# Kernel optimization log

Hardware: AMD Instinct MI355X
Metric: run time of the kernel (lower is better)

The kernel has to match this reference:

```python
import jax, jax.numpy as jnp
import numpy as np
import math

CHANNELS = 128
NUM_NODES = 170
LENGTH = 12
BATCH = 128


def setup_inputs() -> dict:
    key = jax.random.key(0)
    k_x, k_es = jax.random.split(key)
    x = jax.random.normal(k_x, (BATCH, CHANNELS, NUM_NODES, LENGTH), dtype=jnp.float32)
    # xavier_uniform for E_s [channels, num_nodes]
    bound = math.sqrt(6.0 / (CHANNELS + NUM_NODES))
    E_s = jax.random.uniform(k_es, (CHANNELS, NUM_NODES), dtype=jnp.float32,
                             minval=-bound, maxval=bound)
    return {"x": x, "E_s": E_s}


def reference(x, E_s):
    # x: [B, C, N, T], E_s: [C, M] with M == N (num_nodes)
    # Note: the original also computes E_t = x * E_tod**2, which is dead code
    # (never used in the returned value), so it is omitted here.
    C = x.shape[1]
    # node embeddings: sum over channel and time -> [B, N, M]
    E_d = jnp.tanh(jnp.einsum('bcnt,cm->bnm', x, E_s))
    # node-node similarity: contract over the M (embedding) axis -> [B, N, N]
    scores = jax.nn.relu(jnp.einsum('bnm,bkm->bnk', E_d, E_d) / jnp.sqrt(jnp.float32(C)))
    A_adp = jax.nn.softmax(scores, axis=-1)  # [B, N, N]
    A_mean = A_adp.mean(axis=0)              # [N, N]
    return (A_mean > 0.5).astype(jnp.float32)
```

## Files before the change

### kernel.cpp

```cpp
#include <hip/hip_runtime.h>
#include <math.h>

#define NB 128
#define NC 128
#define NN 170
#define NT 12
#define MP 176
#define BSROW 196

#define ESP_SZ (NC * MP)
#define ED_SZ  (NB * NN * MP)
#define P_SZ   (NB * NN * MP)
#define PM_SZ  (8 * NN * NN)

__device__ __forceinline__ float fast_tanh(float x) {
    float cx = fminf(fmaxf(x, -15.f), 15.f);
    float e  = __expf(2.f * cx);
    return (e - 1.f) * __builtin_amdgcn_rcpf(e + 1.f);
}

__global__ __launch_bounds__(256) void k0_pad_es(const float* __restrict__ Es,
                                                 float* __restrict__ Esp) {
    int idx = blockIdx.x * 256 + threadIdx.x;
    if (idx < ESP_SZ) {
        int c = idx / MP, m = idx % MP;
        Esp[idx] = (m < NN) ? Es[c * NN + m] : 0.f;
    }
}

__global__ __launch_bounds__(256) void k2_fused(const float* __restrict__ x,
                                                const float* __restrict__ Esp,
                                                float* __restrict__ Ed) {
    const int b = blockIdx.y, n0 = blockIdx.x * 32;
    const int t = threadIdx.x, tx = t & 15, ty = t >> 4;
    __shared__ __align__(16) float As[16][36];
    __shared__ __align__(16) float Bs[16][BSROW];

    float acc[2][12] = {};
    for (int c0 = 0; c0 < NC; c0 += 16) {
        __syncthreads();
        {
            int c  = t >> 4;
            int nn = (t & 15) * 2;
            #pragma unroll
            for (int u = 0; u < 2; ++u) {
                int n = n0 + nn + u;
                float s = 0.f;
                if (n < NN) {
                    const float4* p = reinterpret_cast<const float4*>(
                        x + ((size_t)((b * NC + c0 + c) * NN) + n) * NT);
                    float4 f0 = p[0], f1 = p[1], f2 = p[2];
                    s = ((f0.x + f0.y) + (f0.z + f0.w))
                      + ((f1.x + f1.y) + (f1.z + f1.w))
                      + ((f2.x + f2.y) + (f2.z + f2.w));
                }
                As[c][nn + u] = s;
            }
        }
        #pragma unroll
        for (int it = 0; it < 3; ++it) {
            int idx = t + it * 256;
            int c = idx / 48, mq = idx - c * 48;
            float4 v = make_float4(0.f, 0.f, 0.f, 0.f);
            if (mq < 44)
                v = *reinterpret_cast<const float4*>(Esp + (c0 + c) * MP + mq * 4);
            *reinterpret_cast<float4*>(&Bs[c][mq * 4]) = v;
        }
        __syncthreads();
        #pragma unroll
        for (int cc = 0; cc < 16; ++cc) {
            float2 av = *reinterpret_cast<const float2*>(&As[cc][ty * 2]);
            float a[2] = {av.x, av.y};
            float bb[12];
            #pragma unroll
            for (int off = 0; off < 3; ++off) {
                float4 bv = *reinterpret_cast<const float4*>(&Bs[cc][tx * 4 + off * 64]);
                bb[off * 4 + 0] = bv.x; bb[off * 4 + 1] = bv.y;
                bb[off * 4 + 2] = bv.z; bb[off * 4 + 3] = bv.w;
            }
            #pragma unroll
            for (int ii = 0; ii < 2; ++ii)
                #pragma unroll
                for (int jj = 0; jj < 12; ++jj)
                    acc[ii][jj] = fmaf(a[ii], bb[jj], acc[ii][jj]);
        }
    }
    #pragma unroll
    for (int ii = 0; ii < 2; ++ii) {
        int n = n0 + ty * 2 + ii;
        if (n >= NN) continue;
        float* Erow = Ed + ((size_t)(b * NN + n)) * MP;
        #pragma unroll
        for (int off = 0; off < 3; ++off) {
            int m = tx * 4 + off * 64;
            if (m >= MP) continue;
            float4 v;
            v.x = fast_tanh(acc[ii][off * 4 + 0]);
            v.y = fast_tanh(acc[ii][off * 4 + 1]);
            v.z = fast_tanh(acc[ii][off * 4 + 2]);
            v.w = fast_tanh(acc[ii][off * 4 + 3]);
            *reinterpret_cast<float4*>(Erow + m) = v;
        }
    }
}

__global__ __launch_bounds__(256) void k3_scores(const float* __restrict__ Ed,
                                                 float* __restrict__ P) {
    const int b = blockIdx.y, r0 = blockIdx.x * 32;
    const int t = threadIdx.x, tx = t & 15, ty = t >> 4;
    __shared__ __align__(16) float Bs[16][BSROW];
    const float* __restrict__ Edb = Ed + (size_t)b * NN * MP;

    float acc[2][12] = {};
    for (int mc = 0; mc < MP; mc += 16) {
        __syncthreads();
        #pragma unroll
        for (int it = 0; it < 3; ++it) {
            int idx = t + it * 256;
            int k = idx >> 2, mq = idx & 3;
            float4 v = make_float4(0.f, 0.f, 0.f, 0.f);
            if (k < NN)
                v = *reinterpret_cast<const float4*>(Edb + (size_t)k * MP + mc + mq * 4);
            Bs[mq * 4 + 0][k] = v.x;
            Bs[mq * 4 + 1][k] = v.y;
            Bs[mq * 4 + 2][k] = v.z;
            Bs[mq * 4 + 3][k] = v.w;
        }
        __syncthreads();
        #pragma unroll
        for (int mm = 0; mm < 16; ++mm) {
            float2 av = *reinterpret_cast<const float2*>(&Bs[mm][r0 + ty * 2]);
            float a[2] = {av.x, av.y};
            float bb[12];
            #pragma unroll
            for (int off = 0; off < 3; ++off) {
                float4 bv = *reinterpret_cast<const float4*>(&Bs[mm][tx * 4 + off * 64]);
                bb[off * 4 + 0] = bv.x; bb[off * 4 + 1] = bv.y;
                bb[off * 4 + 2] = bv.z; bb[off * 4 + 3] = bv.w;
            }
            #pragma unroll
            for (int ii = 0; ii < 2; ++ii)
                #pragma unroll
                for (int jj = 0; jj < 12; ++jj)
                    acc[ii][jj] = fmaf(a[ii], bb[jj], acc[ii][jj]);
        }
    }

    const float scale = 0.08838834764831845f;
    #pragma unroll
    for (int ii = 0; ii < 2; ++ii) {
        int n = r0 + ty * 2 + ii;
        float vv[12];
        float mx = -1.f;
        #pragma unroll
        for (int jj = 0; jj < 12; ++jj) {
            int k = tx * 4 + (jj & 3) + (jj >> 2) * 64;
            float v = fmaxf(acc[ii][jj] * scale, 0.f);
            vv[jj] = (k < NN) ? v : -1.f;
            mx = fmaxf(mx, vv[jj]);
        }
        #pragma unroll
        for (int off = 8; off; off >>= 1) mx = fmaxf(mx, __shfl_xor(mx, off, 64));
        float ex[12], sum = 0.f;
        #pragma unroll
        for (int jj = 0; jj < 12; ++jj) {
            int k = tx * 4 + (jj & 3) + (jj >> 2) * 64;
            float e = (k < NN) ? __expf(vv[jj] - mx) : 0.f;
            ex[jj] = e;
            sum += e;
        }
        #pragma unroll
        for (int off = 8; off; off >>= 1) sum += __shfl_xor(sum, off, 64);
        float inv = 1.f / sum;
        if (n < NN) {
            float* Pr = P + ((size_t)(b * NN + n)) * MP;
            #pragma unroll
            for (int off = 0; off < 3; ++off) {
                int k = tx * 4 + off * 64;
                if (k >= MP) continue;
                float4 v;
                v.x = ex[off * 4 + 0] * inv; v.y = ex[off * 4 + 1] * inv;
                v.z = ex[off * 4 + 2] * inv; v.w = ex[off * 4 + 3] * inv;
                *reinterpret_cast<float4*>(Pr + k) = v;
            }
        }
    }
}

__global__ __launch_bounds__(256) void k4a_partial(const float* __restrict__ P,
                                                   float* __restrict__ Pm) {
    int p = blockIdx.x * 256 + threadIdx.x;
    if (p >= NN * NN) return;
    int n = p / NN, k = p - n * NN;
    const float* base = P + (size_t)blockIdx.y * 16 * NN * MP + (size_t)n * MP + k;
    float s = 0.f;
    #pragma unroll
    for (int b = 0; b < 16; ++b) s += base[(size_t)b * NN * MP];
    Pm[blockIdx.y * (NN * NN) + p] = s;
}

__global__ __launch_bounds__(256) void k4b_thresh(const float* __restrict__ Pm,
                                                  float* __restrict__ out) {
    int p = blockIdx.x * 256 + threadIdx.x;
    if (p >= NN * NN) return;
    float s = 0.f;
    #pragma unroll
    for (int g = 0; g < 8; ++g) s += Pm[g * (NN * NN) + p];
    out[p] = (s * (1.f / 128.f) > 0.5f) ? 1.f : 0.f;
}

extern "C" void kernel_launch(void* const* d_in, const int* in_sizes, int n_in,
                              void* d_out, int out_size, void* d_ws, size_t ws_size,
                              hipStream_t stream) {
    const float* x  = (const float*)d_in[0];
    const float* Es = (const float*)d_in[1];
    float* out = (float*)d_out;
    float* wsf = (float*)d_ws;

    float* Esp = wsf;
    float* Ed  = wsf + ESP_SZ;
    float* P   = wsf + ESP_SZ + ED_SZ;
    float* Pm  = wsf + ESP_SZ + ED_SZ + P_SZ;

    k0_pad_es<<<88, 256, 0, stream>>>(Es, Esp);
    k2_fused<<<dim3(6, 128), 256, 0, stream>>>(x, Esp, Ed);
    k3_scores<<<dim3(6, 128), 256, 0, stream>>>(Ed, P);
    k4a_partial<<<dim3(113, 8), 256, 0, stream>>>(P, Pm);
    k4b_thresh<<<113, 256, 0, stream>>>(Pm, out);
}
```

Measured before the change: 243.7 us.

## Compute similarity scores with fp16 MFMA and row-wise softmax via shared memory

Replaces the FP32 FMA-based E_d·E_dᵀ score kernel with one that converts E_d tiles to fp16 in shared memory and uses 16x16x32 MFMA instructions. Scores are staged in shared memory so each wave runs softmax over whole rows with full-wave shuffles. The aim is to cut the ALU cost of the batched NxN GEMM. The trade-off is fp16 rounding of inputs, which could flip threshold decisions near 0.5, plus extra shared-memory staging.

Measured after the change: 234.7 us. 1.04x faster.

```diff
diff --git a/kernel.cpp b/kernel.cpp
--- a/kernel.cpp
+++ b/kernel.cpp
@@ -12,6 +12,11 @@
 #define ED_SZ  (NB * NN * MP)
 #define P_SZ   (NB * NN * MP)
 #define PM_SZ  (8 * NN * NN)
+
+typedef _Float16 h8 __attribute__((ext_vector_type(8)));
+typedef _Float16 h4 __attribute__((ext_vector_type(4)));
+typedef __fp16   g2 __attribute__((ext_vector_type(2)));
+typedef float    f4 __attribute__((ext_vector_type(4)));
 
 __device__ __forceinline__ float fast_tanh(float x) {
     float cx = fminf(fmaxf(x, -15.f), 15.f);
@@ -104,86 +109,86 @@
     }
 }
 
-__global__ __launch_bounds__(256) void k3_scores(const float* __restrict__ Ed,
-                                                 float* __restrict__ P) {
+__global__ __launch_bounds__(256) void k3_scores_mfma(const float* __restrict__ Ed,
+                                                      float* __restrict__ P) {
     const int b = blockIdx.y, r0 = blockIdx.x * 32;
-    const int t = threadIdx.x, tx = t & 15, ty = t >> 4;
-    __shared__ __align__(16) float Bs[16][BSROW];
+    const int t = threadIdx.x;
+    const int lane = t & 63, wave = t >> 6;
+    const int l15 = lane & 15, quad = lane >> 4;
+
+    __shared__ __align__(16) _Float16 Eh[192 * 40];
+    __shared__ __align__(16) float    Sc[32 * 204];
+
     const float* __restrict__ Edb = Ed + (size_t)b * NN * MP;
 
-    float acc[2][12] = {};
-    for (int mc = 0; mc < MP; mc += 16) {
-        __syncthreads();
-        #pragma unroll
-        for (int it = 0; it < 3; ++it) {
+    f4 acc[2][3] = {};
+    for (int mc = 0; mc < 192; mc += 32) {
+        __syncthreads();
+        #pragma unroll
+        for (int it = 0; it < 6; ++it) {
             int idx = t + it * 256;
-            int k = idx >> 2, mq = idx & 3;
+            int row = idx >> 3, q = idx & 7;
             float4 v = make_float4(0.f, 0.f, 0.f, 0.f);
-            if (k < NN)
-                v = *reinterpret_cast<const float4*>(Edb + (size_t)k * MP + mc + mq * 4);
-            Bs[mq * 4 + 0][k] = v.x;
-            Bs[mq * 4 + 1][k] = v.y;
-            Bs[mq * 4 + 2][k] = v.z;
-            Bs[mq * 4 + 3][k] = v.w;
-        }
-        __syncthreads();
-        #pragma unroll
-        for (int mm = 0; mm < 16; ++mm) {
-            float2 av = *reinterpret_cast<const float2*>(&Bs[mm][r0 + ty * 2]);
-            float a[2] = {av.x, av.y};
-            float bb[12];
-            #pragma unroll
-            for (int off = 0; off < 3; ++off) {
-                float4 bv = *reinterpret_cast<const float4*>(&Bs[mm][tx * 4 + off * 64]);
-                bb[off * 4 + 0] = bv.x; bb[off * 4 + 1] = bv.y;
-                bb[off * 4 + 2] = bv.z; bb[off * 4 + 3] = bv.w;
+            int col = mc + q * 4;
+            if (row < NN && col < MP)
+                v = *reinterpret_cast<const float4*>(Edb + (size_t)row * MP + col);
+            g2 lo = __builtin_amdgcn_cvt_pkrtz(v.x, v.y);
+            g2 hi = __builtin_amdgcn_cvt_pkrtz(v.z, v.w);
+            h4 h;
+            h[0] = (_Float16)lo[0]; h[1] = (_Float16)lo[1];
+            h[2] = (_Float16)hi[0]; h[3] = (_Float16)hi[1];
+            *reinterpret_cast<h4*>(&Eh[row * 40 + q * 4]) = h;
+        }
+        __syncthreads();
+        const int ko = quad * 8;
+        h8 a0 = *reinterpret_cast<const h8*>(&Eh[(r0 + l15) * 40 + ko]);
+        h8 a1 = *reinterpret_cast<const h8*>(&Eh[(r0 + 16 + l15) * 40 + ko]);
+        #pragma unroll
+        for (int ci = 0; ci < 3; ++ci) {
+            int kc = (wave * 3 + ci) * 16 + l15;
+            h8 bf = *reinterpret_cast<const h8*>(&Eh[kc * 40 + ko]);
+            acc[0][ci] = __builtin_amdgcn_mfma_f32_16x16x32_f16(a0, bf, acc[0][ci], 0, 0, 0);
+            acc[1][ci] = __builtin_amdgcn_mfma_f32_16x16x32_f16(a1, bf, acc[1][ci], 0, 0, 0);
+        }
+    }
+
+    const float scale = 0.08838834764831845f;
+    #pragma unroll
+    for (int rt = 0; rt < 2; ++rt)
+        #pragma unroll
+        for (int ci = 0; ci < 3; ++ci) {
+            int col = (wave * 3 + ci) * 16 + l15;
+            #pragma unroll
+            for (int reg = 0; reg < 4; ++reg) {
+                int rloc = rt * 16 + quad * 4 + reg;
+                Sc[rloc * 204 + col] = fmaxf(acc[rt][ci][reg] * scale, 0.f);
             }
-            #pragma unroll
-            for (int ii = 0; ii < 2; ++ii)
-                #pragma unroll
-                for (int jj = 0; jj < 12; ++jj)
-                    acc[ii][jj] = fmaf(a[ii], bb[jj], acc[ii][jj]);
-        }
-    }
-
-    const float scale = 0.08838834764831845f;
-    #pragma unroll
-    for (int ii = 0; ii < 2; ++ii) {
-        int n = r0 + ty * 2 + ii;
-        float vv[12];
-        float mx = -1.f;
-        #pragma unroll
-        for (int jj = 0; jj < 12; ++jj) {
-            int k = tx * 4 + (jj & 3) + (jj >> 2) * 64;
-            float v = fmaxf(acc[ii][jj] * scale, 0.f);
-            vv[jj] = (k < NN) ? v : -1.f;
-            mx = fmaxf(mx, vv[jj]);
-        }
-        #pragma unroll
-        for (int off = 8; off; off >>= 1) mx = fmaxf(mx, __shfl_xor(mx, off, 64));
-        float ex[12], sum = 0.f;
-        #pragma unroll
-        for (int jj = 0; jj < 12; ++jj) {
-            int k = tx * 4 + (jj & 3) + (jj >> 2) * 64;
-            float e = (k < NN) ? __expf(vv[jj] - mx) : 0.f;
-            ex[jj] = e;
-            sum += e;
-        }
-        #pragma unroll
-        for (int off = 8; off; off >>= 1) sum += __shfl_xor(sum, off, 64);
-        float inv = 1.f / sum;
-        if (n < NN) {
-            float* Pr = P + ((size_t)(b * NN + n)) * MP;
-            #pragma unroll
-            for (int off = 0; off < 3; ++off) {
-                int k = tx * 4 + off * 64;
-                if (k >= MP) continue;
-                float4 v;
-                v.x = ex[off * 4 + 0] * inv; v.y = ex[off * 4 + 1] * inv;
-                v.z = ex[off * 4 + 2] * inv; v.w = ex[off * 4 + 3] * inv;
-                *reinterpret_cast<float4*>(Pr + k) = v;
-            }
-        }
+        }
+    __syncthreads();
+
+    for (int rr = 0; rr < 8; ++rr) {
+        int r = wave * 8 + rr;
+        int n = r0 + r;
+        if (n >= NN) continue;
+        float v0 = Sc[r * 204 + lane];
+        float v1 = Sc[r * 204 + lane + 64];
+        int  k2i = lane + 128;
+        bool has2 = (k2i < NN);
+        float v2 = has2 ? Sc[r * 204 + k2i] : -1.f;
+        float m = fmaxf(fmaxf(v0, v1), v2);
+        #pragma unroll
+        for (int off = 32; off; off >>= 1) m = fmaxf(m, __shfl_xor(m, off, 64));
+        float e0 = __expf(v0 - m);
+        float e1 = __expf(v1 - m);
+        float e2 = has2 ? __expf(v2 - m) : 0.f;
+        float s = e0 + e1 + e2;
+        #pragma unroll
+        for (int off = 32; off; off >>= 1) s += __shfl_xor(s, off, 64);
+        float inv = 1.f / s;
+        float* Pr = P + ((size_t)(b * NN + n)) * MP;
+        Pr[lane]      = e0 * inv;
+        Pr[lane + 64] = e1 * inv;
+        if (has2) Pr[k2i] = e2 * inv;
     }
 }
 
@@ -224,7 +229,7 @@
 
     k0_pad_es<<<88, 256, 0, stream>>>(Es, Esp);
     k2_fused<<<dim3(6, 128), 256, 0, stream>>>(x, Esp, Ed);
-    k3_scores<<<dim3(6, 128), 256, 0, stream>>>(Ed, P);
+    k3_scores_mfma<<<dim3(6, 128), 256, 0, stream>>>(Ed, P);
     k4a_partial<<<dim3(113, 8), 256, 0, stream>>>(P, Pm);
     k4b_thresh<<<113, 256, 0, stream>>>(Pm, out);
 }
```
